# Performance work log

Hardware: AMD Instinct MI355X
Metric: run time of the kernel (lower is better)

Reference implementation:

```python
import jax, jax.numpy as jnp
import numpy as np

B, S, E, H = 2, 2048, 1024, 16
D = E // H  # head_dim = 64
SCALE = float(np.sqrt(D))


def setup_inputs() -> dict:
    root = jax.random.key(0)
    ks = jax.random.split(root, 12)
    inp = {
        "query": jax.random.normal(ks[0], (B, S, E), dtype=jnp.float32),
        "key": jax.random.normal(ks[1], (B, S, E), dtype=jnp.float32),
        "value": jax.random.normal(ks[2], (B, S, E), dtype=jnp.float32),
        "mask": jax.random.randint(ks[3], (B, S, S), 0, 2, dtype=jnp.int32),
        # Linear weights stored torch-style as [out, in]; init scale ~ 1/sqrt(E)
        "Wq": jax.random.normal(ks[4], (E, E), dtype=jnp.float32) / np.sqrt(E),
        "bq": jnp.zeros((E,), dtype=jnp.float32),
        "Wk": jax.random.normal(ks[5], (E, E), dtype=jnp.float32) / np.sqrt(E),
        "bk": jnp.zeros((E,), dtype=jnp.float32),
        "Wv": jax.random.normal(ks[6], (E, E), dtype=jnp.float32) / np.sqrt(E),
        "bv": jnp.zeros((E,), dtype=jnp.float32),
        "Wo": jax.random.normal(ks[7], (E, E), dtype=jnp.float32) / np.sqrt(E),
        "bo": jnp.zeros((E,), dtype=jnp.float32),
    }
    return inp


def reference(query, key, value, mask, Wq, bq, Wk, bk, Wv, bv, Wo, bo):
    # Projections (torch Linear: x @ W.T + b)
    Q = query @ Wq.T + bq
    K = key @ Wk.T + bk
    V = value @ Wv.T + bv
    # [B, S, E] -> [B, H, S, D]
    Q = Q.reshape(B, S, H, D).transpose(0, 2, 1, 3)
    K = K.reshape(B, S, H, D).transpose(0, 2, 1, 3)
    V = V.reshape(B, S, H, D).transpose(0, 2, 1, 3)
    # Scaled dot-product scores [B, H, S, S]
    scores = jnp.einsum("bhqd,bhkd->bhqk", Q, K) / SCALE
    # mask==0 positions -> -1e9 (mask broadcast over heads)
    scores = jnp.where(mask[:, None, :, :] == 0, jnp.float32(-1e9), scores)
    attn = jax.nn.softmax(scores, axis=-1)  # dropout is identity in eval
    out = jnp.einsum("bhqk,bhkd->bhqd", attn, V)
    out = out.transpose(0, 2, 1, 3).reshape(B, S, E)
    output = out @ Wo.T + bo
    avg_attn = attn.mean(axis=1)  # [B, S, S]
    return output, avg_attn
```

## Files before the change

kernel.cpp:

```cpp
#include <hip/hip_runtime.h>
#include <stdint.h>

#define BB 2
#define SS 2048
#define EE 1024
#define HH 16
#define DD 64

typedef _Float16 h16;
typedef _Float16 f16x8 __attribute__((ext_vector_type(8)));
typedef _Float16 f16x4 __attribute__((ext_vector_type(4)));
typedef float f32x4 __attribute__((ext_vector_type(4)));

__device__ __forceinline__ void async_ld16(const void* g, void* l) {
  __builtin_amdgcn_global_load_lds((__attribute__((address_space(1))) void*)g,
                                   (__attribute__((address_space(3))) void*)l,
                                   16, 0, 0);
}

__global__ __launch_bounds__(256) void cvt_f16(const float* __restrict__ src,
                                               h16* __restrict__ dst, int n4) {
  int i = blockIdx.x * 256 + threadIdx.x;
  if (i >= n4) return;
  const float4 v = reinterpret_cast<const float4*>(src)[i];
  f16x4 o = {(_Float16)v.x, (_Float16)v.y, (_Float16)v.z, (_Float16)v.w};
  *reinterpret_cast<f16x4*>(dst + i * 4) = o;
}

template <int MODE>
__global__ __launch_bounds__(256, 2) void gemm_bt(const h16* __restrict__ A,
                                                  const h16* __restrict__ Bw,
                                                  const float* __restrict__ bias,
                                                  void* __restrict__ out) {
  constexpr int K = EE;
  __shared__ h16 As[128 * 64];
  __shared__ h16 Bs[64 * 64];
  const int tid = threadIdx.x;
  const int lane = tid & 63, w = tid >> 6;
  const int cg = lane & 15, rg = lane >> 4;
  const int wr = w >> 1, wc = w & 1;
  const int row0 = blockIdx.y * 128, col0 = blockIdx.x * 64;

  f32x4 acc[4][2] = {};

  const h16* Ag = A + row0 * K;
  const h16* Bg = Bw + col0 * K;

  for (int k0 = 0; k0 < K; k0 += 64) {
#pragma unroll
    for (int i = 0; i < 4; ++i) {
      int c = i * 256 + tid;
      async_ld16(Ag + (c >> 3) * K + k0 + (c & 7) * 8,
                 (char*)As + (i * 256 + w * 64) * 16);
    }
#pragma unroll
    for (int i = 0; i < 2; ++i) {
      int c = i * 256 + tid;
      async_ld16(Bg + (c >> 3) * K + k0 + (c & 7) * 8,
                 (char*)Bs + (i * 256 + w * 64) * 16);
    }
    __syncthreads();
#pragma unroll
    for (int kk = 0; kk < 64; kk += 32) {
      f16x8 af[4], bfr[2];
#pragma unroll
      for (int m = 0; m < 4; ++m)
        af[m] = *(const f16x8*)&As[(wr * 64 + m * 16 + cg) * 64 + kk + rg * 8];
#pragma unroll
      for (int n = 0; n < 2; ++n)
        bfr[n] = *(const f16x8*)&Bs[(wc * 32 + n * 16 + cg) * 64 + kk + rg * 8];
#pragma unroll
      for (int m = 0; m < 4; ++m)
#pragma unroll
        for (int n = 0; n < 2; ++n)
          acc[m][n] = __builtin_amdgcn_mfma_f32_16x16x32_f16(af[m], bfr[n], acc[m][n], 0, 0, 0);
    }
    __syncthreads();
  }

#pragma unroll
  for (int n = 0; n < 2; ++n) {
    const int col = col0 + wc * 32 + n * 16 + cg;
    const float bv = bias[col];
#pragma unroll
    for (int m = 0; m < 4; ++m) {
#pragma unroll
      for (int j = 0; j < 4; ++j) {
        const int row = row0 + wr * 64 + m * 16 + rg * 4 + j;
        const float v = acc[m][n][j] + bv;
        if (MODE == 2) {
          ((float*)out)[row * EE + col] = v;
        } else {
          const int b = row >> 11, s = row & (SS - 1);
          const int h = col >> 6, d = col & (DD - 1);
          int idx;
          if (MODE == 0) idx = ((b * HH + h) * SS + s) * DD + d;
          else           idx = ((b * HH + h) * DD + d) * SS + s;
          ((h16*)out)[idx] = (_Float16)v;
        }
      }
    }
  }
}

__global__ __launch_bounds__(256, 2) void attn_fwd(
    const h16* __restrict__ Qh, const h16* __restrict__ Kh, const h16* __restrict__ Vt,
    const int* __restrict__ mask, h16* __restrict__ O,
    float* __restrict__ Mrow, float* __restrict__ Lrow) {
  __shared__ h16 Ks[64 * 64];
  __shared__ h16 Vs[64 * 64];
  __shared__ h16 Ps[4][16][72];
  const int tid = threadIdx.x;
  const int lane = tid & 63, w = tid >> 6;
  const int cg = lane & 15, rg = lane >> 4;
  const int qt = blockIdx.x, bh = blockIdx.y;
  const int b = bh >> 4, h = bh & (HH - 1);
  const int q0 = qt * 64 + w * 16;

  const h16* Qbase = Qh + (bh * SS + q0 + cg) * DD;
  const f16x8 qf0 = *(const f16x8*)(Qbase + rg * 8);
  const f16x8 qf1 = *(const f16x8*)(Qbase + 32 + rg * 8);

  f32x4 o[4] = {};
  float mrun[4] = {-INFINITY, -INFINITY, -INFINITY, -INFINITY};
  float lrun[4] = {0.f, 0.f, 0.f, 0.f};

  const h16* Kg = Kh + bh * SS * DD;
  const h16* Vg = Vt + bh * DD * SS;
  const int* mbase = mask + (b * SS + q0) * SS;

  for (int k0 = 0; k0 < SS; k0 += 64) {
#pragma unroll
    for (int i = 0; i < 2; ++i) {
      int c = i * 256 + tid;
      async_ld16(Kg + (k0 + (c >> 3)) * DD + (c & 7) * 8,
                 (char*)Ks + (i * 256 + w * 64) * 16);
      async_ld16(Vg + (c >> 3) * SS + k0 + (c & 7) * 8,
                 (char*)Vs + (i * 256 + w * 64) * 16);
    }
    __syncthreads();

    f32x4 sc[4];
#pragma unroll
    for (int n = 0; n < 4; ++n) {
      f16x8 kf0 = *(const f16x8*)&Ks[(n * 16 + cg) * 64 + rg * 8];
      f16x8 kf1 = *(const f16x8*)&Ks[(n * 16 + cg) * 64 + 32 + rg * 8];
      f32x4 z = {};
      z = __builtin_amdgcn_mfma_f32_16x16x32_f16(qf0, kf0, z, 0, 0, 0);
      sc[n] = __builtin_amdgcn_mfma_f32_16x16x32_f16(qf1, kf1, z, 0, 0, 0);
    }

#pragma unroll
    for (int j = 0; j < 4; ++j) {
      const int r = rg * 4 + j;
      const int* mrow = mbase + r * SS + k0;
      float v[4];
#pragma unroll
      for (int n = 0; n < 4; ++n)
        v[n] = mrow[n * 16 + cg] ? sc[n][j] * 0.125f : -1e9f;
      float tm = fmaxf(fmaxf(v[0], v[1]), fmaxf(v[2], v[3]));
      tm = fmaxf(tm, __shfl_xor(tm, 1));
      tm = fmaxf(tm, __shfl_xor(tm, 2));
      tm = fmaxf(tm, __shfl_xor(tm, 4));
      tm = fmaxf(tm, __shfl_xor(tm, 8));
      const float mn = fmaxf(mrun[j], tm);
      const float scale = __expf(mrun[j] - mn);
      float ps = 0.f;
#pragma unroll
      for (int n = 0; n < 4; ++n) {
        const float p = __expf(v[n] - mn);
        ps += p;
        Ps[w][r][n * 16 + cg] = (_Float16)p;
      }
      ps += __shfl_xor(ps, 1);
      ps += __shfl_xor(ps, 2);
      ps += __shfl_xor(ps, 4);
      ps += __shfl_xor(ps, 8);
      lrun[j] = lrun[j] * scale + ps;
      mrun[j] = mn;
#pragma unroll
      for (int n = 0; n < 4; ++n) o[n][j] *= scale;
    }
    __syncthreads();

#pragma unroll
    for (int kkb = 0; kkb < 2; ++kkb) {
      f16x8 pa = *(const f16x8*)&Ps[w][cg][kkb * 32 + rg * 8];
#pragma unroll
      for (int n = 0; n < 4; ++n) {
        f16x8 vf = *(const f16x8*)&Vs[(n * 16 + cg) * 64 + kkb * 32 + rg * 8];
        o[n] = __builtin_amdgcn_mfma_f32_16x16x32_f16(pa, vf, o[n], 0, 0, 0);
      }
    }
    __syncthreads();
  }

  float rl[4];
#pragma unroll
  for (int j = 0; j < 4; ++j) rl[j] = 1.f / lrun[j];
#pragma unroll
  for (int n = 0; n < 4; ++n)
#pragma unroll
    for (int j = 0; j < 4; ++j) {
      const int s = q0 + rg * 4 + j;
      O[(b * SS + s) * EE + h * DD + n * 16 + cg] = (_Float16)(o[n][j] * rl[j]);
    }
  if (cg == 0) {
#pragma unroll
    for (int j = 0; j < 4; ++j) {
      const int s = q0 + rg * 4 + j;
      Mrow[bh * SS + s] = mrun[j];
      Lrow[bh * SS + s] = lrun[j];
    }
  }
}

__global__ __launch_bounds__(256, 4) void avg_attn_k(
    const h16* __restrict__ Qh, const h16* __restrict__ Kh,
    const int* __restrict__ mask, const float* __restrict__ Mrow,
    const float* __restrict__ Lrow, float* __restrict__ outAvg) {
  const int tid = threadIdx.x;
  const int lane = tid & 63, w = tid >> 6;
  const int cg = lane & 15, rg = lane >> 4;
  const int kt = blockIdx.x, qt = blockIdx.y, b = blockIdx.z;
  const int q0 = qt * 64 + w * 16, k0 = kt * 64;

  unsigned mbits = 0;
#pragma unroll
  for (int j = 0; j < 4; ++j)
#pragma unroll
    for (int n = 0; n < 4; ++n)
      if (mask[(b * SS + q0 + rg * 4 + j) * SS + k0 + n * 16 + cg])
        mbits |= 1u << (j * 4 + n);

  f32x4 acc[4] = {};
  for (int h = 0; h < HH; ++h) {
    const int bh = b * HH + h;
    const h16* Qb = Qh + (bh * SS + q0 + cg) * DD;
    const f16x8 qf0 = *(const f16x8*)(Qb + rg * 8);
    const f16x8 qf1 = *(const f16x8*)(Qb + 32 + rg * 8);
    const h16* Kb = Kh + (bh * SS + k0) * DD;
    float Mv[4], Rv[4];
#pragma unroll
    for (int j = 0; j < 4; ++j) {
      const int s = q0 + rg * 4 + j;
      Mv[j] = Mrow[bh * SS + s];
      Rv[j] = 1.f / Lrow[bh * SS + s];
    }
#pragma unroll
    for (int n = 0; n < 4; ++n) {
      const f16x8 kf0 = *(const f16x8*)(Kb + (n * 16 + cg) * DD + rg * 8);
      const f16x8 kf1 = *(const f16x8*)(Kb + (n * 16 + cg) * DD + 32 + rg * 8);
      f32x4 z = {};
      z = __builtin_amdgcn_mfma_f32_16x16x32_f16(qf0, kf0, z, 0, 0, 0);
      const f32x4 sc = __builtin_amdgcn_mfma_f32_16x16x32_f16(qf1, kf1, z, 0, 0, 0);
#pragma unroll
      for (int j = 0; j < 4; ++j) {
        const float sv = ((mbits >> (j * 4 + n)) & 1u) ? sc[j] * 0.125f : -1e9f;
        acc[n][j] += __expf(sv - Mv[j]) * Rv[j];
      }
    }
  }
#pragma unroll
  for (int n = 0; n < 4; ++n)
#pragma unroll
    for (int j = 0; j < 4; ++j)
      outAvg[(b * SS + q0 + rg * 4 + j) * SS + k0 + n * 16 + cg] = acc[n][j] * 0.0625f;
}

extern "C" void kernel_launch(void* const* d_in, const int* in_sizes, int n_in,
                              void* d_out, int out_size, void* d_ws, size_t ws_size,
                              hipStream_t stream) {
  const float* query = (const float*)d_in[0];
  const float* key_  = (const float*)d_in[1];
  const float* value = (const float*)d_in[2];
  const int*   mask  = (const int*)d_in[3];
  const float* Wq = (const float*)d_in[4];
  const float* bq = (const float*)d_in[5];
  const float* Wk = (const float*)d_in[6];
  const float* bk = (const float*)d_in[7];
  const float* Wv = (const float*)d_in[8];
  const float* bv = (const float*)d_in[9];
  const float* Wo = (const float*)d_in[10];
  const float* bo = (const float*)d_in[11];

  const size_t SZ_SE = (size_t)BB * SS * EE;
  h16* qx  = (h16*)d_ws;
  h16* kx  = qx + SZ_SE;
  h16* vx  = kx + SZ_SE;
  h16* wqx = vx + SZ_SE;
  h16* wkx = wqx + EE * EE;
  h16* wvx = wkx + EE * EE;
  h16* wox = wvx + EE * EE;
  h16* Qd  = wox + EE * EE;
  h16* Kd  = Qd + SZ_SE;
  h16* Vtd = Kd + SZ_SE;
  h16* Od  = Vtd + SZ_SE;
  float* Mr = (float*)(Od + SZ_SE);
  float* Lr = Mr + (size_t)BB * HH * SS;

  float* outp = (float*)d_out;
  float* avgp = outp + SZ_SE;

  cvt_f16<<<4096, 256, 0, stream>>>(query, qx, (int)(SZ_SE / 4));
  cvt_f16<<<4096, 256, 0, stream>>>(key_,  kx, (int)(SZ_SE / 4));
  cvt_f16<<<4096, 256, 0, stream>>>(value, vx, (int)(SZ_SE / 4));
  cvt_f16<<<1024, 256, 0, stream>>>(Wq, wqx, EE * EE / 4);
  cvt_f16<<<1024, 256, 0, stream>>>(Wk, wkx, EE * EE / 4);
  cvt_f16<<<1024, 256, 0, stream>>>(Wv, wvx, EE * EE / 4);
  cvt_f16<<<1024, 256, 0, stream>>>(Wo, wox, EE * EE / 4);

  gemm_bt<0><<<dim3(16, 32), 256, 0, stream>>>(qx, wqx, bq, Qd);
  gemm_bt<0><<<dim3(16, 32), 256, 0, stream>>>(kx, wkx, bk, Kd);
  gemm_bt<1><<<dim3(16, 32), 256, 0, stream>>>(vx, wvx, bv, Vtd);

  attn_fwd<<<dim3(SS / 64, BB * HH), 256, 0, stream>>>(Qd, Kd, Vtd, mask, Od, Mr, Lr);

  avg_attn_k<<<dim3(SS / 64, SS / 64, BB), 256, 0, stream>>>(Qd, Kd, mask, Mr, Lr, avgp);

  gemm_bt<2><<<dim3(16, 32), 256, 0, stream>>>(Od, wox, bo, outp);
}
```

Measured before the change: 536.4 us.

## Bit-pack mask, use exp2 with folded LSE, drop LDS staging in attention

Adds a ballot-based kernel that packs the int32 mask into 64-bit words, so the attention and averaging kernels read far fewer mask bytes. Softmax switches to exp2 with the 1/sqrt(d)*log2e scale folded into one constant, and the row max and sum are stored as a single log-sum-exp value, which removes a divide per element in avg_attn. attn_fwd now loads K and V fragments straight from global memory instead of staging them through LDS with barriers, and raises its occupancy hint. The conversion launches are merged into grid-y batched kernels. Dropping LDS staging relies on the cache to absorb redundant K/V reads across waves.

```diff
diff --git a/kernel.cpp b/kernel.cpp
--- a/kernel.cpp
+++ b/kernel.cpp
@@ -6,6 +6,7 @@
 #define EE 1024
 #define HH 16
 #define DD 64
+#define C1 0.18033688f
 
 typedef _Float16 h16;
 typedef _Float16 f16x8 __attribute__((ext_vector_type(8)));
@@ -18,13 +19,45 @@
                                    16, 0, 0);
 }
 
-__global__ __launch_bounds__(256) void cvt_f16(const float* __restrict__ src,
-                                               h16* __restrict__ dst, int n4) {
+__global__ __launch_bounds__(256) void cvt_qkv(const float* __restrict__ q,
+                                               const float* __restrict__ k,
+                                               const float* __restrict__ v,
+                                               h16* __restrict__ oq, h16* __restrict__ ok,
+                                               h16* __restrict__ ov, int n4) {
+  const float* s;
+  h16* d;
+  if (blockIdx.y == 0) { s = q; d = oq; }
+  else if (blockIdx.y == 1) { s = k; d = ok; }
+  else { s = v; d = ov; }
   int i = blockIdx.x * 256 + threadIdx.x;
   if (i >= n4) return;
-  const float4 v = reinterpret_cast<const float4*>(src)[i];
-  f16x4 o = {(_Float16)v.x, (_Float16)v.y, (_Float16)v.z, (_Float16)v.w};
-  *reinterpret_cast<f16x4*>(dst + i * 4) = o;
+  const float4 t = reinterpret_cast<const float4*>(s)[i];
+  f16x4 o = {(_Float16)t.x, (_Float16)t.y, (_Float16)t.z, (_Float16)t.w};
+  *reinterpret_cast<f16x4*>(d + i * 4) = o;
+}
+
+__global__ __launch_bounds__(256) void cvt_w4(const float* __restrict__ w0, const float* __restrict__ w1,
+                                              const float* __restrict__ w2, const float* __restrict__ w3,
+                                              h16* __restrict__ o0, h16* __restrict__ o1,
+                                              h16* __restrict__ o2, h16* __restrict__ o3, int n4) {
+  const float* s;
+  h16* d;
+  if (blockIdx.y == 0) { s = w0; d = o0; }
+  else if (blockIdx.y == 1) { s = w1; d = o1; }
+  else if (blockIdx.y == 2) { s = w2; d = o2; }
+  else { s = w3; d = o3; }
+  int i = blockIdx.x * 256 + threadIdx.x;
+  if (i >= n4) return;
+  const float4 t = reinterpret_cast<const float4*>(s)[i];
+  f16x4 o = {(_Float16)t.x, (_Float16)t.y, (_Float16)t.z, (_Float16)t.w};
+  *reinterpret_cast<f16x4*>(d + i * 4) = o;
+}
+
+__global__ __launch_bounds__(256) void pack_mask(const int* __restrict__ mask,
+                                                 unsigned long long* __restrict__ pk) {
+  const size_t i = (size_t)blockIdx.x * 256 + threadIdx.x;
+  const unsigned long long b = __ballot(mask[i] != 0);
+  if ((threadIdx.x & 63) == 0) pk[i >> 6] = b;
 }
 
 template <int MODE>
@@ -103,12 +136,9 @@
   }
 }
 
-__global__ __launch_bounds__(256, 2) void attn_fwd(
+__global__ __launch_bounds__(256, 4) void attn_fwd(
     const h16* __restrict__ Qh, const h16* __restrict__ Kh, const h16* __restrict__ Vt,
-    const int* __restrict__ mask, h16* __restrict__ O,
-    float* __restrict__ Mrow, float* __restrict__ Lrow) {
-  __shared__ h16 Ks[64 * 64];
-  __shared__ h16 Vs[64 * 64];
+    const uint2* __restrict__ mpk, h16* __restrict__ O, float* __restrict__ Crow) {
   __shared__ h16 Ps[4][16][72];
   const int tid = threadIdx.x;
   const int lane = tid & 63, w = tid >> 6;
@@ -117,7 +147,7 @@
   const int b = bh >> 4, h = bh & (HH - 1);
   const int q0 = qt * 64 + w * 16;
 
-  const h16* Qbase = Qh + (bh * SS + q0 + cg) * DD;
+  const h16* Qbase = Qh + ((size_t)bh * SS + q0 + cg) * DD;
   const f16x8 qf0 = *(const f16x8*)(Qbase + rg * 8);
   const f16x8 qf1 = *(const f16x8*)(Qbase + 32 + rg * 8);
 
@@ -125,50 +155,55 @@
   float mrun[4] = {-INFINITY, -INFINITY, -INFINITY, -INFINITY};
   float lrun[4] = {0.f, 0.f, 0.f, 0.f};
 
-  const h16* Kg = Kh + bh * SS * DD;
-  const h16* Vg = Vt + bh * DD * SS;
-  const int* mbase = mask + (b * SS + q0) * SS;
+  const h16* Kg = Kh + (size_t)bh * SS * DD;
+  const h16* Vg = Vt + (size_t)bh * DD * SS;
+  const uint2* mb = mpk + ((size_t)b * SS + q0) * (SS / 64);
 
   for (int k0 = 0; k0 < SS; k0 += 64) {
-#pragma unroll
-    for (int i = 0; i < 2; ++i) {
-      int c = i * 256 + tid;
-      async_ld16(Kg + (k0 + (c >> 3)) * DD + (c & 7) * 8,
-                 (char*)Ks + (i * 256 + w * 64) * 16);
-      async_ld16(Vg + (c >> 3) * SS + k0 + (c & 7) * 8,
-                 (char*)Vs + (i * 256 + w * 64) * 16);
-    }
-    __syncthreads();
-
+    const int kc = k0 >> 6;
     f32x4 sc[4];
 #pragma unroll
     for (int n = 0; n < 4; ++n) {
-      f16x8 kf0 = *(const f16x8*)&Ks[(n * 16 + cg) * 64 + rg * 8];
-      f16x8 kf1 = *(const f16x8*)&Ks[(n * 16 + cg) * 64 + 32 + rg * 8];
+      const h16* kr = Kg + (size_t)(k0 + n * 16 + cg) * DD + rg * 8;
+      const f16x8 kf0 = *(const f16x8*)kr;
+      const f16x8 kf1 = *(const f16x8*)(kr + 32);
       f32x4 z = {};
       z = __builtin_amdgcn_mfma_f32_16x16x32_f16(qf0, kf0, z, 0, 0, 0);
       sc[n] = __builtin_amdgcn_mfma_f32_16x16x32_f16(qf1, kf1, z, 0, 0, 0);
     }
 
+    f16x8 vf[4][2];
+#pragma unroll
+    for (int n = 0; n < 4; ++n) {
+      const h16* vr = Vg + (size_t)(n * 16 + cg) * SS + k0 + rg * 8;
+      vf[n][0] = *(const f16x8*)vr;
+      vf[n][1] = *(const f16x8*)(vr + 32);
+    }
+
+    float scl[4];
 #pragma unroll
     for (int j = 0; j < 4; ++j) {
       const int r = rg * 4 + j;
-      const int* mrow = mbase + r * SS + k0;
+      const uint2 pk = mb[r * (SS / 64) + kc];
       float v[4];
 #pragma unroll
-      for (int n = 0; n < 4; ++n)
-        v[n] = mrow[n * 16 + cg] ? sc[n][j] * 0.125f : -1e9f;
+      for (int n = 0; n < 4; ++n) {
+        const unsigned wbits = (n & 2) ? pk.y : pk.x;
+        const bool on = (wbits >> ((n & 1) * 16 + cg)) & 1u;
+        v[n] = on ? sc[n][j] * C1 : -1e9f;
+      }
       float tm = fmaxf(fmaxf(v[0], v[1]), fmaxf(v[2], v[3]));
       tm = fmaxf(tm, __shfl_xor(tm, 1));
       tm = fmaxf(tm, __shfl_xor(tm, 2));
       tm = fmaxf(tm, __shfl_xor(tm, 4));
       tm = fmaxf(tm, __shfl_xor(tm, 8));
       const float mn = fmaxf(mrun[j], tm);
-      const float scale = __expf(mrun[j] - mn);
+      scl[j] = exp2f(mrun[j] - mn);
+      mrun[j] = mn;
       float ps = 0.f;
 #pragma unroll
       for (int n = 0; n < 4; ++n) {
-        const float p = __expf(v[n] - mn);
+        const float p = exp2f(v[n] - mn);
         ps += p;
         Ps[w][r][n * 16 + cg] = (_Float16)p;
       }
@@ -176,23 +211,20 @@
       ps += __shfl_xor(ps, 2);
       ps += __shfl_xor(ps, 4);
       ps += __shfl_xor(ps, 8);
-      lrun[j] = lrun[j] * scale + ps;
-      mrun[j] = mn;
-#pragma unroll
-      for (int n = 0; n < 4; ++n) o[n][j] *= scale;
-    }
-    __syncthreads();
+      lrun[j] = lrun[j] * scl[j] + ps;
+    }
+#pragma unroll
+    for (int n = 0; n < 4; ++n)
+#pragma unroll
+      for (int j = 0; j < 4; ++j) o[n][j] *= scl[j];
 
 #pragma unroll
     for (int kkb = 0; kkb < 2; ++kkb) {
-      f16x8 pa = *(const f16x8*)&Ps[w][cg][kkb * 32 + rg * 8];
-#pragma unroll
-      for (int n = 0; n < 4; ++n) {
-        f16x8 vf = *(const f16x8*)&Vs[(n * 16 + cg) * 64 + kkb * 32 + rg * 8];
-        o[n] = __builtin_amdgcn_mfma_f32_16x16x32_f16(pa, vf, o[n], 0, 0, 0);
-      }
-    }
-    __syncthreads();
+      const f16x8 pa = *(const f16x8*)&Ps[w][cg][kkb * 32 + rg * 8];
+#pragma unroll
+      for (int n = 0; n < 4; ++n)
+        o[n] = __builtin_amdgcn_mfma_f32_16x16x32_f16(pa, vf[n][kkb], o[n], 0, 0, 0);
+    }
   }
 
   float rl[4];
@@ -203,22 +235,21 @@
 #pragma unroll
     for (int j = 0; j < 4; ++j) {
       const int s = q0 + rg * 4 + j;
-      O[(b * SS + s) * EE + h * DD + n * 16 + cg] = (_Float16)(o[n][j] * rl[j]);
+      O[((size_t)b * SS + s) * EE + h * DD + n * 16 + cg] = (_Float16)(o[n][j] * rl[j]);
     }
   if (cg == 0) {
 #pragma unroll
     for (int j = 0; j < 4; ++j) {
       const int s = q0 + rg * 4 + j;
-      Mrow[bh * SS + s] = mrun[j];
-      Lrow[bh * SS + s] = lrun[j];
+      Crow[(size_t)bh * SS + s] = mrun[j] + __log2f(lrun[j]);
     }
   }
 }
 
 __global__ __launch_bounds__(256, 4) void avg_attn_k(
     const h16* __restrict__ Qh, const h16* __restrict__ Kh,
-    const int* __restrict__ mask, const float* __restrict__ Mrow,
-    const float* __restrict__ Lrow, float* __restrict__ outAvg) {
+    const uint2* __restrict__ mpk, const float* __restrict__ Crow,
+    float* __restrict__ outAvg) {
   const int tid = threadIdx.x;
   const int lane = tid & 63, w = tid >> 6;
   const int cg = lane & 15, rg = lane >> 4;
@@ -227,37 +258,38 @@
 
   unsigned mbits = 0;
 #pragma unroll
-  for (int j = 0; j < 4; ++j)
-#pragma unroll
-    for (int n = 0; n < 4; ++n)
-      if (mask[(b * SS + q0 + rg * 4 + j) * SS + k0 + n * 16 + cg])
-        mbits |= 1u << (j * 4 + n);
+  for (int j = 0; j < 4; ++j) {
+    const uint2 pk = mpk[((size_t)b * SS + q0 + rg * 4 + j) * (SS / 64) + kt];
+#pragma unroll
+    for (int n = 0; n < 4; ++n) {
+      const unsigned wbits = (n & 2) ? pk.y : pk.x;
+      mbits |= ((wbits >> ((n & 1) * 16 + cg)) & 1u) << (j * 4 + n);
+    }
+  }
 
   f32x4 acc[4] = {};
+#pragma unroll 2
   for (int h = 0; h < HH; ++h) {
     const int bh = b * HH + h;
-    const h16* Qb = Qh + (bh * SS + q0 + cg) * DD;
+    const h16* Qb = Qh + ((size_t)bh * SS + q0 + cg) * DD;
     const f16x8 qf0 = *(const f16x8*)(Qb + rg * 8);
     const f16x8 qf1 = *(const f16x8*)(Qb + 32 + rg * 8);
-    const h16* Kb = Kh + (bh * SS + k0) * DD;
-    float Mv[4], Rv[4];
-#pragma unroll
-    for (int j = 0; j < 4; ++j) {
-      const int s = q0 + rg * 4 + j;
-      Mv[j] = Mrow[bh * SS + s];
-      Rv[j] = 1.f / Lrow[bh * SS + s];
-    }
+    const h16* Kb = Kh + ((size_t)bh * SS + k0) * DD;
+    float Cm[4];
+#pragma unroll
+    for (int j = 0; j < 4; ++j) Cm[j] = Crow[(size_t)bh * SS + q0 + rg * 4 + j];
 #pragma unroll
     for (int n = 0; n < 4; ++n) {
-      const f16x8 kf0 = *(const f16x8*)(Kb + (n * 16 + cg) * DD + rg * 8);
-      const f16x8 kf1 = *(const f16x8*)(Kb + (n * 16 + cg) * DD + 32 + rg * 8);
+      const h16* kr = Kb + (size_t)(n * 16 + cg) * DD + rg * 8;
+      const f16x8 kf0 = *(const f16x8*)kr;
+      const f16x8 kf1 = *(const f16x8*)(kr + 32);
       f32x4 z = {};
       z = __builtin_amdgcn_mfma_f32_16x16x32_f16(qf0, kf0, z, 0, 0, 0);
       const f32x4 sc = __builtin_amdgcn_mfma_f32_16x16x32_f16(qf1, kf1, z, 0, 0, 0);
 #pragma unroll
       for (int j = 0; j < 4; ++j) {
-        const float sv = ((mbits >> (j * 4 + n)) & 1u) ? sc[j] * 0.125f : -1e9f;
-        acc[n][j] += __expf(sv - Mv[j]) * Rv[j];
+        const float t = ((mbits >> (j * 4 + n)) & 1u) ? sc[j] * C1 : -1e9f;
+        acc[n][j] += exp2f(t - Cm[j]);
       }
     }
   }
@@ -265,7 +297,7 @@
   for (int n = 0; n < 4; ++n)
 #pragma unroll
     for (int j = 0; j < 4; ++j)
-      outAvg[(b * SS + q0 + rg * 4 + j) * SS + k0 + n * 16 + cg] = acc[n][j] * 0.0625f;
+      outAvg[((size_t)b * SS + q0 + rg * 4 + j) * SS + k0 + n * 16 + cg] = acc[n][j] * 0.0625f;
 }
 
 extern "C" void kernel_launch(void* const* d_in, const int* in_sizes, int n_in,
@@ -296,27 +328,23 @@
   h16* Kd  = Qd + SZ_SE;
   h16* Vtd = Kd + SZ_SE;
   h16* Od  = Vtd + SZ_SE;
-  float* Mr = (float*)(Od + SZ_SE);
-  float* Lr = Mr + (size_t)BB * HH * SS;
+  float* Cr = (float*)(Od + SZ_SE);
+  unsigned long long* mpk = (unsigned long long*)(Cr + (size_t)BB * HH * SS);
 
   float* outp = (float*)d_out;
   float* avgp = outp + SZ_SE;
 
-  cvt_f16<<<4096, 256, 0, stream>>>(query, qx, (int)(SZ_SE / 4));
-  cvt_f16<<<4096, 256, 0, stream>>>(key_,  kx, (int)(SZ_SE / 4));
-  cvt_f16<<<4096, 256, 0, stream>>>(value, vx, (int)(SZ_SE / 4));
-  cvt_f16<<<1024, 256, 0, stream>>>(Wq, wqx, EE * EE / 4);
-  cvt_f16<<<1024, 256, 0, stream>>>(Wk, wkx, EE * EE / 4);
-  cvt_f16<<<1024, 256, 0, stream>>>(Wv, wvx, EE * EE / 4);
-  cvt_f16<<<1024, 256, 0, stream>>>(Wo, wox, EE * EE / 4);
+  pack_mask<<<(BB * SS * SS) / 256, 256, 0, stream>>>(mask, mpk);
+  cvt_qkv<<<dim3(4096, 3), 256, 0, stream>>>(query, key_, value, qx, kx, vx, (int)(SZ_SE / 4));
+  cvt_w4<<<dim3(1024, 4), 256, 0, stream>>>(Wq, Wk, Wv, Wo, wqx, wkx, wvx, wox, EE * EE / 4);
 
   gemm_bt<0><<<dim3(16, 32), 256, 0, stream>>>(qx, wqx, bq, Qd);
   gemm_bt<0><<<dim3(16, 32), 256, 0, stream>>>(kx, wkx, bk, Kd);
   gemm_bt<1><<<dim3(16, 32), 256, 0, stream>>>(vx, wvx, bv, Vtd);
 
-  attn_fwd<<<dim3(SS / 64, BB * HH), 256, 0, stream>>>(Qd, Kd, Vtd, mask, Od, Mr, Lr);
-
-  avg_attn_k<<<dim3(SS / 64, SS / 64, BB), 256, 0, stream>>>(Qd, Kd, mask, Mr, Lr, avgp);
+  attn_fwd<<<dim3(SS / 64, BB * HH), 256, 0, stream>>>(Qd, Kd, Vtd, (const uint2*)mpk, Od, Cr);
+
+  avg_attn_k<<<dim3(SS / 64, SS / 64, BB), 256, 0, stream>>>(Qd, Kd, (const uint2*)mpk, Cr, avgp);
 
   gemm_bt<2><<<dim3(16, 32), 256, 0, stream>>>(Od, wox, bo, outp);
 }
```

Measured after the change: 640.1 us. +19.3%, slower.
